# Performance work log

Measured on AMD Instinct MI355X. Metric: run time of the kernel, lower is better.

## Reference

```python
import jax, jax.numpy as jnp
import numpy as np

NEG_SLOPE = 0.2
EPS = 1e-16


def gat_conv(x, edge_index, W, att_src, att_dst, bias, heads, out_ch, concat):
    """PyG-style GATConv (eval mode, add_self_loops=True)."""
    N = x.shape[0]
    h = (x @ W).reshape(N, heads, out_ch)              # [N,H,C]
    loop = jnp.arange(N, dtype=edge_index.dtype)
    src = jnp.concatenate([edge_index[0], loop])       # [E+N]
    dst = jnp.concatenate([edge_index[1], loop])
    a_src = jnp.sum(h * att_src, axis=-1)              # [N,H]
    a_dst = jnp.sum(h * att_dst, axis=-1)
    e = jax.nn.leaky_relu(a_src[src] + a_dst[dst], NEG_SLOPE)  # [E+N,H]
    # segment softmax over destination nodes
    m = jax.ops.segment_max(e, dst, num_segments=N)
    e = jnp.exp(e - m[dst])
    s = jax.ops.segment_sum(e, dst, num_segments=N)
    alpha = e / (s[dst] + EPS)                         # [E+N,H]
    msg = h[src] * alpha[..., None]                    # [E+N,H,C]
    out = jax.ops.segment_sum(msg, dst, num_segments=N)  # [N,H,C]
    out = out.reshape(N, heads * out_ch) if concat else out.mean(axis=1)
    return out + bias


def setup_inputs() -> dict:
    key = jax.random.key(0)
    ks = jax.random.split(key, 11)
    N, F, E = 100000, 128, 1600000
    H1, C1 = 4, 16
    H2, C2 = 1, 16
    return {
        "x": jax.random.normal(ks[0], (N, F), dtype=jnp.float32),
        "edge_index": jax.random.randint(ks[1], (2, E), 0, N, dtype=jnp.int64) if jax.config.jax_enable_x64 else jax.random.randint(ks[1], (2, E), 0, N).astype(jnp.int32),
        "W1": jax.random.normal(ks[2], (F, H1 * C1), dtype=jnp.float32) * 0.1,
        "att_src1": jax.random.normal(ks[3], (H1, C1), dtype=jnp.float32) * 0.1,
        "att_dst1": jax.random.normal(ks[4], (H1, C1), dtype=jnp.float32) * 0.1,
        "bias1": jax.random.normal(ks[5], (H1 * C1,), dtype=jnp.float32) * 0.1,
        "W2": jax.random.normal(ks[6], (H1 * C1, H2 * C2), dtype=jnp.float32) * 0.1,
        "att_src2": jax.random.normal(ks[7], (H2, C2), dtype=jnp.float32) * 0.1,
        "att_dst2": jax.random.normal(ks[8], (H2, C2), dtype=jnp.float32) * 0.1,
        "bias2": jax.random.normal(ks[9], (C2,), dtype=jnp.float32) * 0.1,
    }


def reference(x, edge_index, W1, att_src1, att_dst1, bias1, W2, att_src2, att_dst2, bias2):
    # dropout is identity in eval mode
    h = gat_conv(x, edge_index, W1, att_src1, att_dst1, bias1, heads=4, out_ch=16, concat=True)
    h = jax.nn.elu(h)
    h = gat_conv(h, edge_index, W2, att_src2, att_dst2, bias2, heads=1, out_ch=16, concat=False)
    return jax.nn.log_softmax(h, axis=1)
```

## Files before the change

### kernel.cpp

```cpp
#include <hip/hip_runtime.h>
#include <hip/hip_fp16.h>
#include <hip/hip_bf16.h>
#include <math.h>


#define LRELU(v) ((v) > 0.f ? (v) : 0.2f * (v))
#define BSH 8
#define BCAP 5120
#define CHK 8192

typedef __attribute__((ext_vector_type(8))) short short8;
typedef __attribute__((ext_vector_type(8))) _Float16 half8;
typedef __attribute__((ext_vector_type(4))) _Float16 half4;
typedef __attribute__((ext_vector_type(4))) float float4v;

static __device__ __forceinline__ short f2bf(float f) {
    __hip_bfloat16 b = __float2bfloat16(f);
    return *reinterpret_cast<short*>(&b);
}

__global__ __launch_bounds__(256) void k_pre(const int* __restrict__ ei, int* __restrict__ cursor,
                                             int* __restrict__ stage, int E, int NBK,
                                             const float* __restrict__ x,
                                             const float* __restrict__ W1,
                                             const float* __restrict__ att_src1,
                                             const float* __restrict__ att_dst1,
                                             __half* __restrict__ h1,
                                             float* __restrict__ a_src, float* __restrict__ a_dst,
                                             int N, int GS) {
    __shared__ __align__(16) char smem[80 * 136 * 2];
    int tid = threadIdx.x;
    if (blockIdx.x < GS) {
        int* hist = (int*)smem;
        int* cnt2 = hist + 512;
        int* base = cnt2 + 512;
        int e0 = blockIdx.x * CHK;
        int nedge = E - e0; if (nedge > CHK) nedge = CHK;
        for (int i = tid; i < 512; i += 256) { hist[i] = 0; cnt2[i] = 0; }
        __syncthreads();
        for (int j = tid; j < nedge; j += 256) {
            int d = ei[E + e0 + j];
            atomicAdd(&hist[d >> BSH], 1);
        }
        __syncthreads();
        for (int b = tid; b < NBK; b += 256) {
            int c = hist[b];
            if (c > 0) base[b] = b * BCAP + atomicAdd(&cursor[b], c);
        }
        __syncthreads();
        for (int j = tid; j < nedge; j += 256) {
            int s = ei[e0 + j];
            int d = ei[E + e0 + j];
            int b = d >> BSH;
            int r = atomicAdd(&cnt2[b], 1);
            stage[base[b] + r] = s | ((d & ((1 << BSH) - 1)) << 17);
        }
    } else {
        short* wt = (short*)smem;
        for (int i = tid; i < 128 * 64; i += 256) {
            int k = i >> 6, c = i & 63;
            wt[c * 136 + k] = f2bf(W1[i]);
        }
        for (int i = tid; i < 16 * 128; i += 256) {
            int col = i >> 7, k = i & 127;
            float v = 0.f;
            if (col < 8) {
                int h = col & 3;
                const float* att = (col < 4) ? att_src1 : att_dst1;
                #pragma unroll
                for (int c = 0; c < 16; c++) v += W1[k * 64 + h * 16 + c] * att[h * 16 + c];
            }
            wt[(64 + col) * 136 + k] = f2bf(v);
        }
        __syncthreads();
        int wave = tid >> 6, lane = tid & 63;
        int m = lane & 15, q = lane >> 4;
        int nbase = (blockIdx.x - GS) * 64 + wave * 16;
        int anode = nbase + m;
        bool rowok = anode < N;
        const float* xrow = x + (size_t)(rowok ? anode : 0) * 128 + q * 8;

        float4v acc[5];
        #pragma unroll
        for (int ct = 0; ct < 5; ct++)
            #pragma unroll
            for (int r = 0; r < 4; r++) acc[ct][r] = 0.f;

        #pragma unroll
        for (int kc = 0; kc < 4; kc++) {
            float4 u0 = make_float4(0.f, 0.f, 0.f, 0.f), u1 = u0;
            if (rowok) {
                u0 = *(const float4*)(xrow + kc * 32);
                u1 = *(const float4*)(xrow + kc * 32 + 4);
            }
            short8 af;
            af[0] = f2bf(u0.x); af[1] = f2bf(u0.y); af[2] = f2bf(u0.z); af[3] = f2bf(u0.w);
            af[4] = f2bf(u1.x); af[5] = f2bf(u1.y); af[6] = f2bf(u1.z); af[7] = f2bf(u1.w);
            #pragma unroll
            for (int ct = 0; ct < 5; ct++) {
                short8 bf = *(const short8*)&wt[(ct * 16 + m) * 136 + kc * 32 + q * 8];
                acc[ct] = __builtin_amdgcn_mfma_f32_16x16x32_bf16(af, bf, acc[ct], 0, 0, 0);
            }
        }
        #pragma unroll
        for (int ct = 0; ct < 4; ct++) {
            #pragma unroll
            for (int r = 0; r < 4; r++) {
                int n = nbase + q * 4 + r;
                if (n < N) h1[(size_t)n * 64 + ct * 16 + m] = __float2half(acc[ct][r]);
            }
        }
        #pragma unroll
        for (int r = 0; r < 4; r++) {
            int n = nbase + q * 4 + r;
            if (n < N) {
                float v = acc[4][r];
                if (m < 4) a_src[n * 4 + m] = v;
                else if (m < 8) a_dst[n * 4 + (m - 4)] = v;
            }
        }
    }
}

__global__ __launch_bounds__(256) void k_build(const int* __restrict__ stage,
                                               const int* __restrict__ cursor,
                                               int* __restrict__ row_start,
                                               int* __restrict__ csr,
                                               int NBK, int E, int N) {
    __shared__ int cnt[256];
    __shared__ int lb[256];
    __shared__ int cur[256];
    __shared__ int sA[256];
    int b = blockIdx.x, tid = threadIdx.x;
    int nodes0 = b << BSH;
    int nnodes = N - nodes0; if (nnodes > 256) nnodes = 256;
    int partial = 0;
    for (int i = tid; i < b; i += 256) partial += cursor[i];
    sA[tid] = partial;
    __syncthreads();
    for (int off = 128; off >= 1; off >>= 1) {
        if (tid < off) sA[tid] += sA[tid + off];
        __syncthreads();
    }
    int ebase = sA[0];
    int ecnt = cursor[b];
    __syncthreads();
    if (b == 0 && tid == 0) row_start[N] = E + N;
    const int* sbk = stage + b * BCAP;
    cnt[tid] = (tid < nnodes) ? 1 : 0;
    __syncthreads();
    for (int e = tid; e < ecnt; e += 256) {
        int l = (sbk[e] >> 17) & 255;
        atomicAdd(&cnt[l], 1);
    }
    __syncthreads();
    int myc = cnt[tid];
    sA[tid] = myc;
    __syncthreads();
    for (int off = 1; off < 256; off <<= 1) {
        int r = sA[tid] + ((tid >= off) ? sA[tid - off] : 0);
        __syncthreads();
        sA[tid] = r;
        __syncthreads();
    }
    int gb = ebase + nodes0;
    lb[tid] = sA[tid] - myc;
    cur[tid] = 1;
    __syncthreads();
    if (tid < nnodes) {
        row_start[nodes0 + tid] = gb + lb[tid];
        csr[gb + lb[tid]] = nodes0 + tid;
    }
    __syncthreads();
    for (int e = tid; e < ecnt; e += 256) {
        int v = sbk[e];
        int l = (v >> 17) & 255;
        int src = v & 0x1FFFF;
        int r = atomicAdd(&cur[l], 1);
        csr[gb + lb[l] + r] = src;
    }
}

__global__ __launch_bounds__(256) void k_agg1f(const int* __restrict__ row_start,
                                               const int* __restrict__ csr_src,
                                               const float* __restrict__ a_src,
                                               const float* __restrict__ a_dst,
                                               const __half* __restrict__ h1,
                                               const float* __restrict__ bias,
                                               const float* __restrict__ W2,
                                               const float* __restrict__ att_src2,
                                               const float* __restrict__ att_dst2,
                                               __half* __restrict__ h2,
                                               float* __restrict__ a_src2,
                                               float* __restrict__ a_dst2, int N) {
    __shared__ float sW2[64 * 16];
    __shared__ float sAs[16], sAd[16];
    int tid = threadIdx.x;
    for (int i = tid; i < 1024; i += 256) sW2[i] = W2[i];
    if (tid < 16) { sAs[tid] = att_src2[tid]; sAd[tid] = att_dst2[tid]; }
    __syncthreads();
    int wave = tid >> 6, lane = tid & 63;
    int grp = lane >> 3, sub = lane & 3, par = (lane >> 2) & 1;
    int node = blockIdx.x * 32 + wave * 8 + grp;
    if (node >= N) return;
    int row = row_start[node];
    int deg = row_start[node + 1] - row;
    float adm = a_dst[node * 4 + sub];
    const _Float16* hb = (const _Float16*)h1 + sub * 16;
    const int* cp = csr_src + row + par;
    float A[16];
    #pragma unroll
    for (int c = 0; c < 16; c++) A[c] = 0.f;
    float sh = 0.f;
    int c0 = 0, c1 = 0, c2 = 0, c3 = 0;
    if (deg >= 8) { c0 = cp[0]; c1 = cp[2]; c2 = cp[4]; c3 = cp[6]; }
    int j = 0;
    for (; j + 8 <= deg; j += 8) {
        int s0 = c0, s1 = c1, s2 = c2, s3 = c3;
        float x0 = a_src[s0 * 4 + sub] + adm;
        float x1 = a_src[s1 * 4 + sub] + adm;
        float x2 = a_src[s2 * 4 + sub] + adm;
        float x3 = a_src[s3 * 4 + sub] + adm;
        half8 p0 = *(const half8*)(hb + (size_t)s0 * 64);
        half8 q0 = *(const half8*)(hb + (size_t)s0 * 64 + 8);
        half8 p1 = *(const half8*)(hb + (size_t)s1 * 64);
        half8 q1 = *(const half8*)(hb + (size_t)s1 * 64 + 8);
        half8 p2 = *(const half8*)(hb + (size_t)s2 * 64);
        half8 q2 = *(const half8*)(hb + (size_t)s2 * 64 + 8);
        half8 p3 = *(const half8*)(hb + (size_t)s3 * 64);
        half8 q3 = *(const half8*)(hb + (size_t)s3 * 64 + 8);
        if (j + 16 <= deg) {
            c0 = cp[j + 8]; c1 = cp[j + 10]; c2 = cp[j + 12]; c3 = cp[j + 14];
        }
        float e0 = __expf(fmaxf(x0, 0.2f * x0));
        float e1 = __expf(fmaxf(x1, 0.2f * x1));
        float e2 = __expf(fmaxf(x2, 0.2f * x2));
        float e3 = __expf(fmaxf(x3, 0.2f * x3));
        sh += (e0 + e1) + (e2 + e3);
        #pragma unroll
        for (int c = 0; c < 8; c++) {
            A[c]     += e0 * (float)p0[c] + e1 * (float)p1[c]
                      + e2 * (float)p2[c] + e3 * (float)p3[c];
            A[c + 8] += e0 * (float)q0[c] + e1 * (float)q1[c]
                      + e2 * (float)q2[c] + e3 * (float)q3[c];
        }
    }
    for (; j < deg; j += 2) {
        int idx = j + par;
        if (idx < deg) {
            int s = csr_src[row + idx];
            float xv = a_src[s * 4 + sub] + adm;
            half8 p = *(const half8*)(hb + (size_t)s * 64);
            half8 q = *(const half8*)(hb + (size_t)s * 64 + 8);
            float e = __expf(fmaxf(xv, 0.2f * xv));
            sh += e;
            #pragma unroll
            for (int c = 0; c < 8; c++) {
                A[c]     += e * (float)p[c];
                A[c + 8] += e * (float)q[c];
            }
        }
    }
    sh += __shfl_xor(sh, 4, 64);
    #pragma unroll
    for (int c = 0; c < 16; c++) A[c] += __shfl_xor(A[c], 4, 64);
    float iv = 1.f / (sh + 1e-16f);
    const float4* bb = (const float4*)bias + sub * 4;
    float o[16];
    #pragma unroll
    for (int c4 = 0; c4 < 4; c4++) {
        float4 b = bb[c4];
        float o0 = A[c4 * 4 + 0] * iv + b.x;
        float o1 = A[c4 * 4 + 1] * iv + b.y;
        float o2 = A[c4 * 4 + 2] * iv + b.z;
        float o3 = A[c4 * 4 + 3] * iv + b.w;
        o[c4 * 4 + 0] = (o0 > 0.f) ? o0 : (__expf(o0) - 1.f);
        o[c4 * 4 + 1] = (o1 > 0.f) ? o1 : (__expf(o1) - 1.f);
        o[c4 * 4 + 2] = (o2 > 0.f) ? o2 : (__expf(o2) - 1.f);
        o[c4 * 4 + 3] = (o3 > 0.f) ? o3 : (__expf(o3) - 1.f);
    }
    float pk[8];
    #pragma unroll
    for (int kk = 0; kk < 8; kk++) pk[kk] = 0.f;
    #pragma unroll
    for (int cc = 0; cc < 16; cc++) {
        float ov = o[cc];
        const float* wr = &sW2[(sub * 16 + cc) * 16 + par * 8];
        #pragma unroll
        for (int kk = 0; kk < 8; kk++) pk[kk] += ov * wr[kk];
    }
    #pragma unroll
    for (int kk = 0; kk < 8; kk++) {
        pk[kk] += __shfl_xor(pk[kk], 1, 64);
        pk[kk] += __shfl_xor(pk[kk], 2, 64);
    }
    if (sub == 0) {
        union { __half2 hh[4]; float4 f; } u;
        u.hh[0] = __floats2half2_rn(pk[0], pk[1]);
        u.hh[1] = __floats2half2_rn(pk[2], pk[3]);
        u.hh[2] = __floats2half2_rn(pk[4], pk[5]);
        u.hh[3] = __floats2half2_rn(pk[6], pk[7]);
        *(float4*)&h2[(size_t)node * 16 + par * 8] = u.f;
    }
    float ps = 0.f, pd = 0.f;
    #pragma unroll
    for (int kk = 0; kk < 8; kk++) {
        ps += pk[kk] * sAs[par * 8 + kk];
        pd += pk[kk] * sAd[par * 8 + kk];
    }
    ps += __shfl_xor(ps, 4, 64);
    pd += __shfl_xor(pd, 4, 64);
    if (sub == 0 && par == 0) { a_src2[node] = ps; a_dst2[node] = pd; }
}

__global__ __launch_bounds__(256) void k_agg2(const int* __restrict__ row_start,
                                              const int* __restrict__ csr_src,
                                              const float* __restrict__ a_src,
                                              const float* __restrict__ a_dst,
                                              const __half* __restrict__ h2,
                                              const float* __restrict__ bias,
                                              float* __restrict__ out, int N) {
    int tid = threadIdx.x;
    int wave = tid >> 6, lane = tid & 63;
    int grp = lane >> 4, sub = lane & 3, par = (lane >> 2) & 3;
    int node = blockIdx.x * 16 + wave * 4 + grp;
    if (node >= N) return;
    int row = row_start[node];
    int deg = row_start[node + 1] - row;
    float ad = a_dst[node];
    const _Float16* hb = (const _Float16*)h2 + sub * 4;
    const int* cp = csr_src + row + par;
    float A0 = 0.f, A1 = 0.f, A2 = 0.f, A3 = 0.f;
    float sh = 0.f;
    int c0 = 0, c1 = 0, c2 = 0, c3 = 0;
    if (deg >= 16) { c0 = cp[0]; c1 = cp[4]; c2 = cp[8]; c3 = cp[12]; }
    int j = 0;
    for (; j + 16 <= deg; j += 16) {
        int s0 = c0, s1 = c1, s2 = c2, s3 = c3;
        float x0 = a_src[s0] + ad;
        float x1 = a_src[s1] + ad;
        float x2 = a_src[s2] + ad;
        float x3 = a_src[s3] + ad;
        half4 v0 = *(const half4*)(hb + (size_t)s0 * 16);
        half4 v1 = *(const half4*)(hb + (size_t)s1 * 16);
        half4 v2 = *(const half4*)(hb + (size_t)s2 * 16);
        half4 v3 = *(const half4*)(hb + (size_t)s3 * 16);
        if (j + 32 <= deg) {
            c0 = cp[j + 16]; c1 = cp[j + 20]; c2 = cp[j + 24]; c3 = cp[j + 28];
        }
        float e0 = __expf(fmaxf(x0, 0.2f * x0));
        float e1 = __expf(fmaxf(x1, 0.2f * x1));
        float e2 = __expf(fmaxf(x2, 0.2f * x2));
        float e3 = __expf(fmaxf(x3, 0.2f * x3));
        sh += (e0 + e1) + (e2 + e3);
        A0 += e0 * (float)v0[0] + e1 * (float)v1[0] + e2 * (float)v2[0] + e3 * (float)v3[0];
        A1 += e0 * (float)v0[1] + e1 * (float)v1[1] + e2 * (float)v2[1] + e3 * (float)v3[1];
        A2 += e0 * (float)v0[2] + e1 * (float)v1[2] + e2 * (float)v2[2] + e3 * (float)v3[2];
        A3 += e0 * (float)v0[3] + e1 * (float)v1[3] + e2 * (float)v2[3] + e3 * (float)v3[3];
    }
    for (; j < deg; j += 4) {
        int idx = j + par;
        if (idx < deg) {
            int s = csr_src[row + idx];
            float xv = a_src[s] + ad;
            half4 v = *(const half4*)(hb + (size_t)s * 16);
            float e = __expf(fmaxf(xv, 0.2f * xv));
            sh += e;
            A0 += e * (float)v[0];
            A1 += e * (float)v[1];
            A2 += e * (float)v[2];
            A3 += e * (float)v[3];
        }
    }
    sh += __shfl_xor(sh, 4, 64);  sh += __shfl_xor(sh, 8, 64);
    A0 += __shfl_xor(A0, 4, 64);  A0 += __shfl_xor(A0, 8, 64);
    A1 += __shfl_xor(A1, 4, 64);  A1 += __shfl_xor(A1, 8, 64);
    A2 += __shfl_xor(A2, 4, 64);  A2 += __shfl_xor(A2, 8, 64);
    A3 += __shfl_xor(A3, 4, 64);  A3 += __shfl_xor(A3, 8, 64);
    float iv = 1.f / (sh + 1e-16f);
    float4 b = ((const float4*)bias)[sub];
    float v0 = A0 * iv + b.x;
    float v1 = A1 * iv + b.y;
    float v2 = A2 * iv + b.z;
    float v3 = A3 * iv + b.w;
    float mx = fmaxf(fmaxf(v0, v1), fmaxf(v2, v3));
    mx = fmaxf(mx, __shfl_xor(mx, 1, 64));
    mx = fmaxf(mx, __shfl_xor(mx, 2, 64));
    float se = __expf(v0 - mx) + __expf(v1 - mx) + __expf(v2 - mx) + __expf(v3 - mx);
    se += __shfl_xor(se, 1, 64);
    se += __shfl_xor(se, 2, 64);
    float ls = mx + __logf(se);
    if (par == 0)
        *(float4*)&out[(size_t)node * 16 + sub * 4] =
            make_float4(v0 - ls, v1 - ls, v2 - ls, v3 - ls);
}

extern "C" void kernel_launch(void* const* d_in, const int* in_sizes, int n_in,
                              void* d_out, int out_size, void* d_ws, size_t ws_size,
                              hipStream_t stream) {
    const float* x        = (const float*)d_in[0];
    const int*   ei       = (const int*)d_in[1];
    const float* W1       = (const float*)d_in[2];
    const float* att_src1 = (const float*)d_in[3];
    const float* att_dst1 = (const float*)d_in[4];
    const float* bias1    = (const float*)d_in[5];
    const float* W2       = (const float*)d_in[6];
    const float* att_src2 = (const float*)d_in[7];
    const float* att_dst2 = (const float*)d_in[8];
    const float* bias2    = (const float*)d_in[9];
    float* out = (float*)d_out;

    const int N = in_sizes[0] / 128;
    const int E = in_sizes[1] / 2;
    const int NBK = (N + 255) >> BSH;
    const int GS = (E + CHK - 1) / CHK;
    const int GG = (N + 63) / 64;

    char* p = (char*)d_ws;
    auto alloc = [&](size_t bytes) -> void* {
        void* r = (void*)p;
        p += (bytes + 255) & ~(size_t)255;
        return r;
    };
    __half* h1     = (__half*)alloc((size_t)N * 64 * 2);
    __half* h2     = (__half*)alloc((size_t)N * 16 * 2);
    float* a_src1  = (float*)alloc((size_t)N * 4 * 4);
    float* a_dst1  = (float*)alloc((size_t)N * 4 * 4);
    float* a_src2  = (float*)alloc((size_t)N * 4);
    float* a_dst2  = (float*)alloc((size_t)N * 4);
    int*   row_st  = (int*)alloc((size_t)(N + 1) * 4);
    int*   csr     = (int*)alloc((size_t)(E + N) * 4);
    int*   stage   = (int*)alloc((size_t)NBK * BCAP * 4);
    int*   cursor  = (int*)alloc((size_t)NBK * 4);
    (void)ws_size; (void)n_in; (void)out_size;

    hipMemsetAsync(cursor, 0, (size_t)NBK * 4, stream);
    k_pre<<<GS + GG, 256, 0, stream>>>(ei, cursor, stage, E, NBK,
                                       x, W1, att_src1, att_dst1,
                                       h1, a_src1, a_dst1, N, GS);
    k_build<<<NBK, 256, 0, stream>>>(stage, cursor, row_st, csr, NBK, E, N);
    k_agg1f<<<(N + 31) / 32, 256, 0, stream>>>(row_st, csr, a_src1, a_dst1, h1, bias1,
                                               W2, att_src2, att_dst2,
                                               h2, a_src2, a_dst2, N);
    k_agg2<<<(N + 15) / 16, 256, 0, stream>>>(row_st, csr, a_src2, a_dst2, h2, bias2, out, N);
}
```

Measured before the change: 229.9 us.

## Precompute bf16 weight tile once, vectorize edge bucketing, remap agg2 lanes

```diff
diff --git a/kernel.cpp b/kernel.cpp
--- a/kernel.cpp
+++ b/kernel.cpp
@@ -4,10 +4,9 @@
 #include <math.h>
 
 
-#define LRELU(v) ((v) > 0.f ? (v) : 0.2f * (v))
 #define BSH 8
 #define BCAP 5120
-#define CHK 8192
+#define CHK 4096
 
 typedef __attribute__((ext_vector_type(8))) short short8;
 typedef __attribute__((ext_vector_type(8))) _Float16 half8;
@@ -19,12 +18,37 @@
     return *reinterpret_cast<short*>(&b);
 }
 
+__global__ __launch_bounds__(256) void k_init(int* __restrict__ cursor, int NBK,
+                                              const float* __restrict__ W1,
+                                              const float* __restrict__ att_src1,
+                                              const float* __restrict__ att_dst1,
+                                              short* __restrict__ wtg) {
+    int tid = threadIdx.x;
+    if (blockIdx.x == 0) {
+        for (int i = tid; i < NBK; i += 256) cursor[i] = 0;
+    } else {
+        for (int i = tid; i < 128 * 64; i += 256) {
+            int k = i >> 6, c = i & 63;
+            wtg[c * 136 + k] = f2bf(W1[i]);
+        }
+        for (int i = tid; i < 16 * 128; i += 256) {
+            int col = i >> 7, k = i & 127;
+            float v = 0.f;
+            if (col < 8) {
+                int h = col & 3;
+                const float* att = (col < 4) ? att_src1 : att_dst1;
+                #pragma unroll
+                for (int c = 0; c < 16; c++) v += W1[k * 64 + h * 16 + c] * att[h * 16 + c];
+            }
+            wtg[(64 + col) * 136 + k] = f2bf(v);
+        }
+    }
+}
+
 __global__ __launch_bounds__(256) void k_pre(const int* __restrict__ ei, int* __restrict__ cursor,
                                              int* __restrict__ stage, int E, int NBK,
                                              const float* __restrict__ x,
-                                             const float* __restrict__ W1,
-                                             const float* __restrict__ att_src1,
-                                             const float* __restrict__ att_dst1,
+                                             const short* __restrict__ wtg,
                                              __half* __restrict__ h1,
                                              float* __restrict__ a_src, float* __restrict__ a_dst,
                                              int N, int GS) {
@@ -36,41 +60,52 @@
         int* base = cnt2 + 512;
         int e0 = blockIdx.x * CHK;
         int nedge = E - e0; if (nedge > CHK) nedge = CHK;
+        int nv4 = nedge >> 2, rem = nedge & 3;
+        const int4* dv4 = (const int4*)(ei + E + e0);
+        const int4* sv4 = (const int4*)(ei + e0);
         for (int i = tid; i < 512; i += 256) { hist[i] = 0; cnt2[i] = 0; }
         __syncthreads();
-        for (int j = tid; j < nedge; j += 256) {
-            int d = ei[E + e0 + j];
-            atomicAdd(&hist[d >> BSH], 1);
-        }
+        for (int i = tid; i < nv4; i += 256) {
+            int4 d = dv4[i];
+            atomicAdd(&hist[d.x >> BSH], 1);
+            atomicAdd(&hist[d.y >> BSH], 1);
+            atomicAdd(&hist[d.z >> BSH], 1);
+            atomicAdd(&hist[d.w >> BSH], 1);
+        }
+        if (tid < rem) atomicAdd(&hist[ei[E + e0 + nv4 * 4 + tid] >> BSH], 1);
         __syncthreads();
         for (int b = tid; b < NBK; b += 256) {
             int c = hist[b];
             if (c > 0) base[b] = b * BCAP + atomicAdd(&cursor[b], c);
         }
         __syncthreads();
-        for (int j = tid; j < nedge; j += 256) {
-            int s = ei[e0 + j];
-            int d = ei[E + e0 + j];
+        for (int i = tid; i < nv4; i += 256) {
+            int4 s = sv4[i];
+            int4 d = dv4[i];
+            int b, r;
+            b = d.x >> BSH; r = atomicAdd(&cnt2[b], 1);
+            stage[base[b] + r] = s.x | ((d.x & 255) << 17);
+            b = d.y >> BSH; r = atomicAdd(&cnt2[b], 1);
+            stage[base[b] + r] = s.y | ((d.y & 255) << 17);
+            b = d.z >> BSH; r = atomicAdd(&cnt2[b], 1);
+            stage[base[b] + r] = s.z | ((d.z & 255) << 17);
+            b = d.w >> BSH; r = atomicAdd(&cnt2[b], 1);
+            stage[base[b] + r] = s.w | ((d.w & 255) << 17);
+        }
+        if (tid < rem) {
+            int e = nv4 * 4 + tid;
+            int s = ei[e0 + e];
+            int d = ei[E + e0 + e];
             int b = d >> BSH;
             int r = atomicAdd(&cnt2[b], 1);
-            stage[base[b] + r] = s | ((d & ((1 << BSH) - 1)) << 17);
+            stage[base[b] + r] = s | ((d & 255) << 17);
         }
     } else {
         short* wt = (short*)smem;
-        for (int i = tid; i < 128 * 64; i += 256) {
-            int k = i >> 6, c = i & 63;
-            wt[c * 136 + k] = f2bf(W1[i]);
-        }
-        for (int i = tid; i < 16 * 128; i += 256) {
-            int col = i >> 7, k = i & 127;
-            float v = 0.f;
-            if (col < 8) {
-                int h = col & 3;
-                const float* att = (col < 4) ? att_src1 : att_dst1;
-                #pragma unroll
-                for (int c = 0; c < 16; c++) v += W1[k * 64 + h * 16 + c] * att[h * 16 + c];
-            }
-            wt[(64 + col) * 136 + k] = f2bf(v);
+        {
+            int4* wd = (int4*)wt;
+            const int4* ws = (const int4*)wtg;
+            for (int i = tid; i < (80 * 136 * 2) / 16; i += 256) wd[i] = ws[i];
         }
         __syncthreads();
         int wave = tid >> 6, lane = tid & 63;
@@ -149,10 +184,15 @@
     const int* sbk = stage + b * BCAP;
     cnt[tid] = (tid < nnodes) ? 1 : 0;
     __syncthreads();
-    for (int e = tid; e < ecnt; e += 256) {
-        int l = (sbk[e] >> 17) & 255;
-        atomicAdd(&cnt[l], 1);
-    }
+    int e4 = ecnt & ~3;
+    for (int e = tid * 4; e < e4; e += 1024) {
+        int4 v = *(const int4*)&sbk[e];
+        atomicAdd(&cnt[(v.x >> 17) & 255], 1);
+        atomicAdd(&cnt[(v.y >> 17) & 255], 1);
+        atomicAdd(&cnt[(v.z >> 17) & 255], 1);
+        atomicAdd(&cnt[(v.w >> 17) & 255], 1);
+    }
+    if (tid < (ecnt & 3)) atomicAdd(&cnt[(sbk[e4 + tid] >> 17) & 255], 1);
     __syncthreads();
     int myc = cnt[tid];
     sA[tid] = myc;
@@ -172,12 +212,19 @@
         csr[gb + lb[tid]] = nodes0 + tid;
     }
     __syncthreads();
-    for (int e = tid; e < ecnt; e += 256) {
-        int v = sbk[e];
+    for (int e = tid * 4; e < e4; e += 1024) {
+        int4 v = *(const int4*)&sbk[e];
+        int l, r;
+        l = (v.x >> 17) & 255; r = atomicAdd(&cur[l], 1); csr[gb + lb[l] + r] = v.x & 0x1FFFF;
+        l = (v.y >> 17) & 255; r = atomicAdd(&cur[l], 1); csr[gb + lb[l] + r] = v.y & 0x1FFFF;
+        l = (v.z >> 17) & 255; r = atomicAdd(&cur[l], 1); csr[gb + lb[l] + r] = v.z & 0x1FFFF;
+        l = (v.w >> 17) & 255; r = atomicAdd(&cur[l], 1); csr[gb + lb[l] + r] = v.w & 0x1FFFF;
+    }
+    if (tid < (ecnt & 3)) {
+        int v = sbk[e4 + tid];
         int l = (v >> 17) & 255;
-        int src = v & 0x1FFFF;
         int r = atomicAdd(&cur[l], 1);
-        csr[gb + lb[l] + r] = src;
+        csr[gb + lb[l] + r] = v & 0x1FFFF;
     }
 }
 
@@ -193,10 +240,10 @@
                                                __half* __restrict__ h2,
                                                float* __restrict__ a_src2,
                                                float* __restrict__ a_dst2, int N) {
-    __shared__ float sW2[64 * 16];
+    __shared__ float sW2[64 * 17];
     __shared__ float sAs[16], sAd[16];
     int tid = threadIdx.x;
-    for (int i = tid; i < 1024; i += 256) sW2[i] = W2[i];
+    for (int i = tid; i < 1024; i += 256) sW2[(i >> 4) * 17 + (i & 15)] = W2[i];
     if (tid < 16) { sAs[tid] = att_src2[tid]; sAd[tid] = att_dst2[tid]; }
     __syncthreads();
     int wave = tid >> 6, lane = tid & 63;
@@ -285,7 +332,7 @@
     #pragma unroll
     for (int cc = 0; cc < 16; cc++) {
         float ov = o[cc];
-        const float* wr = &sW2[(sub * 16 + cc) * 16 + par * 8];
+        const float* wr = &sW2[(sub * 16 + cc) * 17 + par * 8];
         #pragma unroll
         for (int kk = 0; kk < 8; kk++) pk[kk] += ov * wr[kk];
     }
@@ -322,8 +369,8 @@
                                               float* __restrict__ out, int N) {
     int tid = threadIdx.x;
     int wave = tid >> 6, lane = tid & 63;
-    int grp = lane >> 4, sub = lane & 3, par = (lane >> 2) & 3;
-    int node = blockIdx.x * 16 + wave * 4 + grp;
+    int grp = lane >> 3, sub = lane & 3, par = (lane >> 2) & 1;
+    int node = blockIdx.x * 32 + wave * 8 + grp;
     if (node >= N) return;
     int row = row_start[node];
     int deg = row_start[node + 1] - row;
@@ -333,9 +380,9 @@
     float A0 = 0.f, A1 = 0.f, A2 = 0.f, A3 = 0.f;
     float sh = 0.f;
     int c0 = 0, c1 = 0, c2 = 0, c3 = 0;
-    if (deg >= 16) { c0 = cp[0]; c1 = cp[4]; c2 = cp[8]; c3 = cp[12]; }
+    if (deg >= 8) { c0 = cp[0]; c1 = cp[2]; c2 = cp[4]; c3 = cp[6]; }
     int j = 0;
-    for (; j + 16 <= deg; j += 16) {
+    for (; j + 8 <= deg; j += 8) {
         int s0 = c0, s1 = c1, s2 = c2, s3 = c3;
         float x0 = a_src[s0] + ad;
         float x1 = a_src[s1] + ad;
@@ -345,8 +392,8 @@
         half4 v1 = *(const half4*)(hb + (size_t)s1 * 16);
         half4 v2 = *(const half4*)(hb + (size_t)s2 * 16);
         half4 v3 = *(const half4*)(hb + (size_t)s3 * 16);
-        if (j + 32 <= deg) {
-            c0 = cp[j + 16]; c1 = cp[j + 20]; c2 = cp[j + 24]; c3 = cp[j + 28];
+        if (j + 16 <= deg) {
+            c0 = cp[j + 8]; c1 = cp[j + 10]; c2 = cp[j + 12]; c3 = cp[j + 14];
         }
         float e0 = __expf(fmaxf(x0, 0.2f * x0));
         float e1 = __expf(fmaxf(x1, 0.2f * x1));
@@ -358,7 +405,7 @@
         A2 += e0 * (float)v0[2] + e1 * (float)v1[2] + e2 * (float)v2[2] + e3 * (float)v3[2];
         A3 += e0 * (float)v0[3] + e1 * (float)v1[3] + e2 * (float)v2[3] + e3 * (float)v3[3];
     }
-    for (; j < deg; j += 4) {
+    for (; j < deg; j += 2) {
         int idx = j + par;
         if (idx < deg) {
             int s = csr_src[row + idx];
@@ -372,11 +419,11 @@
             A3 += e * (float)v[3];
         }
     }
-    sh += __shfl_xor(sh, 4, 64);  sh += __shfl_xor(sh, 8, 64);
-    A0 += __shfl_xor(A0, 4, 64);  A0 += __shfl_xor(A0, 8, 64);
-    A1 += __shfl_xor(A1, 4, 64);  A1 += __shfl_xor(A1, 8, 64);
-    A2 += __shfl_xor(A2, 4, 64);  A2 += __shfl_xor(A2, 8, 64);
-    A3 += __shfl_xor(A3, 4, 64);  A3 += __shfl_xor(A3, 8, 64);
+    sh += __shfl_xor(sh, 4, 64);
+    A0 += __shfl_xor(A0, 4, 64);
+    A1 += __shfl_xor(A1, 4, 64);
+    A2 += __shfl_xor(A2, 4, 64);
+    A3 += __shfl_xor(A3, 4, 64);
     float iv = 1.f / (sh + 1e-16f);
     float4 b = ((const float4*)bias)[sub];
     float v0 = A0 * iv + b.x;
@@ -432,15 +479,15 @@
     int*   csr     = (int*)alloc((size_t)(E + N) * 4);
     int*   stage   = (int*)alloc((size_t)NBK * BCAP * 4);
     int*   cursor  = (int*)alloc((size_t)NBK * 4);
+    short* wtg     = (short*)alloc(80 * 136 * 2);
     (void)ws_size; (void)n_in; (void)out_size;
 
-    hipMemsetAsync(cursor, 0, (size_t)NBK * 4, stream);
+    k_init<<<2, 256, 0, stream>>>(cursor, NBK, W1, att_src1, att_dst1, wtg);
     k_pre<<<GS + GG, 256, 0, stream>>>(ei, cursor, stage, E, NBK,
-                                       x, W1, att_src1, att_dst1,
-                                       h1, a_src1, a_dst1, N, GS);
+                                       x, wtg, h1, a_src1, a_dst1, N, GS);
     k_build<<<NBK, 256, 0, stream>>>(stage, cursor, row_st, csr, NBK, E, N);
     k_agg1f<<<(N + 31) / 32, 256, 0, stream>>>(row_st, csr, a_src1, a_dst1, h1, bias1,
                                                W2, att_src2, att_dst2,
                                                h2, a_src2, a_dst2, N);
-    k_agg2<<<(N + 15) / 16, 256, 0, stream>>>(row_st, csr, a_src2, a_dst2, h2, bias2, out, N);
-}
+    k_agg2<<<(N + 31) / 32, 256, 0, stream>>>(row_st, csr, a_src2, a_dst2, h2, bias2, out, N);
+}
```

New measurement: 230.0 us. Within noise of the previous version (+0.1%).
